# Kernel tuning notes

Measured on AMD Instinct MI355X. Metric: run time of the kernel, lower is better.

## Reference

```python
import jax, jax.numpy as jnp
import numpy as np

B, D, F, P = 65536, 256, 512, 256


def setup_inputs() -> dict:
    key = jax.random.key(0)
    k_x, k_f, k_p, k_a, k_b, k_t = jax.random.split(key, 6)
    x = jax.random.normal(k_x, (B, D), dtype=jnp.float32)
    # reset_parameters: uniform(-0.27, 1)
    features = jax.random.uniform(k_f, (F, D), dtype=jnp.float32, minval=-0.27, maxval=1.0)
    prototypes = jax.random.uniform(k_p, (P, D), dtype=jnp.float32, minval=-0.27, maxval=1.0)
    # alpha/beta/theta init to zeros in the module; use small random values so the
    # output is non-trivial for kernel correctness checking.
    alpha = jax.random.normal(k_a, (1,), dtype=jnp.float32) * 0.1
    beta = jax.random.normal(k_b, (1,), dtype=jnp.float32) * 0.1
    theta = jax.random.normal(k_t, (1,), dtype=jnp.float32) * 0.1
    return {"x": x, "features": features, "prototypes": prototypes,
            "alpha": alpha, "beta": beta, "theta": theta}


def reference(x, features, prototypes, alpha, beta, theta):
    # Shared projections
    x_features = x @ features.T                 # [B, F]
    p_features = prototypes @ features.T        # [P, F]
    x_present = jax.nn.relu(x_features)         # [B, F]
    p_present = jax.nn.relu(p_features)         # [P, F]
    x_weighted = x_features * x_present         # [B, F]
    p_weighted = p_features * p_present         # [P, F]

    # Tversky terms
    common = x_weighted @ p_weighted.T                          # [B, P]
    x_weighted_sum = jnp.sum(x_weighted, axis=1, keepdims=True)  # [B, 1]
    x_p_interaction = x_weighted @ p_present.T                  # [B, P]
    x_distinctive = x_weighted_sum - x_p_interaction            # [B, P]
    p_weighted_sum = jnp.sum(p_weighted, axis=1)[None, :]        # [1, P]
    x_p_weighted_interaction = x_present @ p_weighted.T         # [B, P]
    p_distinctive = p_weighted_sum - x_p_weighted_interaction   # [B, P]

    return theta * common - alpha * x_distinctive - beta * p_distinctive
```

## Files before the change

kernel.cpp:

```cpp
#include <hip/hip_runtime.h>
#include <cstdint>
#include <cstddef>

#define Bsz 65536
#define Dsz 256
#define Fsz 512
#define Psz 256

typedef __attribute__((ext_vector_type(8))) short short8;
typedef __attribute__((ext_vector_type(4))) short short4v;
typedef __attribute__((ext_vector_type(4))) float float4v;
typedef __attribute__((ext_vector_type(16))) float float16v;

__device__ inline short f2bf(float f) {
    unsigned u = __builtin_bit_cast(unsigned, f);
    u = (u + 0x7FFFu + ((u >> 16) & 1u)) >> 16;
    return (short)u;
}
__device__ inline float bf2f(short s) {
    unsigned u = ((unsigned)(unsigned short)s) << 16;
    return __builtin_bit_cast(float, u);
}
__device__ inline void async16(const void* g, void* l) {
    __builtin_amdgcn_global_load_lds((const __attribute__((address_space(1))) void*)g,
                                     (__attribute__((address_space(3))) void*)l, 16, 0, 0);
}

__global__ void k_prep(const float* __restrict__ features, short* __restrict__ featb,
                       float* __restrict__ pws_neg) {
    int i = blockIdx.x * 256 + threadIdx.x;
    featb[i] = f2bf(features[i]);
    if (blockIdx.x == 0) pws_neg[threadIdx.x] = 0.f;
}

#define SBPITCH 136

__global__ __launch_bounds__(256, 2) void k_pside(
    const float* __restrict__ prototypes, const short* __restrict__ featb,
    const float* __restrict__ beta_p,
    short* __restrict__ pwt, short* __restrict__ ppm1t, float* __restrict__ pws_neg)
{
    __shared__ char lds[35840];
    short* As = (short*)lds;
    short* Bs = (short*)(lds + 16384);
    short* Sb = (short*)lds;

    const int t = threadIdx.x;
    const int w = t >> 6, lane = t & 63, l15 = lane & 15, l4 = lane >> 4;
    const int rowg = blockIdx.x >> 2, nc = blockIdx.x & 3;
    const float beta = *beta_p;

    float4v acc[4][4];
    #pragma unroll
    for (int a = 0; a < 4; ++a)
        #pragma unroll
        for (int b = 0; b < 4; ++b) acc[a][b] = (float4v){0.f, 0.f, 0.f, 0.f};

    const float* pbase = prototypes + (size_t)rowg * 128 * Dsz;

    for (int kc = 0; kc < 4; ++kc) {
        __syncthreads();
        #pragma unroll
        for (int j = 0; j < 8; ++j) {
            int idx = j * 1024 + t * 4;
            int r = idx >> 6, c = idx & 63;
            float4v v = *(const float4v*)(pbase + (size_t)r * Dsz + kc * 64 + c);
            int unit = r * 8 + ((c >> 3) ^ (r & 7));
            short4v s; s.x = f2bf(v.x); s.y = f2bf(v.y); s.z = f2bf(v.z); s.w = f2bf(v.w);
            *(short4v*)((char*)As + unit * 16 + (c & 7) * 2) = s;
        }
        #pragma unroll
        for (int j = 0; j < 4; ++j) {
            int u0 = j * 256 + w * 64;
            int u = u0 + lane;
            int m = u >> 3, k8 = (u & 7) ^ (m & 7);
            async16(featb + (size_t)(nc * 128 + m) * Dsz + kc * 64 + k8 * 8, Bs + (size_t)u0 * 8);
        }
        __syncthreads();
        #pragma unroll
        for (int kk = 0; kk < 2; ++kk) {
            short8 af[4], bf[4];
            const int k8 = kk * 4 + l4;
            #pragma unroll
            for (int tm = 0; tm < 4; ++tm) {
                int m = (w & 1) * 64 + tm * 16 + l15;
                af[tm] = *(const short8*)&As[(m * 8 + (k8 ^ (m & 7))) * 8];
            }
            #pragma unroll
            for (int tn = 0; tn < 4; ++tn) {
                int n = (w >> 1) * 64 + tn * 16 + l15;
                bf[tn] = *(const short8*)&Bs[(n * 8 + (k8 ^ (n & 7))) * 8];
            }
            #pragma unroll
            for (int tm = 0; tm < 4; ++tm)
                #pragma unroll
                for (int tn = 0; tn < 4; ++tn)
                    acc[tm][tn] = __builtin_amdgcn_mfma_f32_16x16x32_bf16(af[tm], bf[tn], acc[tm][tn], 0, 0, 0);
        }
    }
    __syncthreads();
    #pragma unroll
    for (int tm = 0; tm < 4; ++tm)
        #pragma unroll
        for (int tn = 0; tn < 4; ++tn)
            #pragma unroll
            for (int r = 0; r < 4; ++r) {
                int row = (w & 1) * 64 + tm * 16 + l4 * 4 + r;
                int col = (w >> 1) * 64 + tn * 16 + l15;
                Sb[row * SBPITCH + col] = f2bf(acc[tm][tn][r]);
            }
    __syncthreads();
    #pragma unroll
    for (int rep = 0; rep < 8; ++rep) {
        int u = rep * 256 + t;
        int row = u >> 4, i = u & 15;
        short8 sv = *(const short8*)&Sb[row * SBPITCH + i * 8];
        short8 pwv, pmv;
        float sum = 0.f;
        #pragma unroll
        for (int e = 0; e < 8; ++e) {
            float pf = bf2f(sv[e]);
            float pp = fmaxf(pf, 0.f);
            float pw = pf * pp;
            pwv[e] = f2bf(pw);
            pmv[e] = f2bf(pp - 1.0f);
            sum += pw;
        }
        size_t p = (size_t)rowg * 128 + row;
        int gcol = nc * 128 + i * 8;
        *(short8*)&pwt[p * Fsz + gcol]   = pwv;
        *(short8*)&ppm1t[p * Fsz + gcol] = pmv;
        #pragma unroll
        for (int mk = 1; mk < 16; mk <<= 1) sum += __shfl_xor(sum, mk, 64);
        if ((lane & 15) == 0) atomicAdd(&pws_neg[p], -beta * sum);
    }
}

__global__ __launch_bounds__(256, 3) void k_main(
    const float* __restrict__ x, const short* __restrict__ featb,
    const short* __restrict__ pwt, const short* __restrict__ ppm1t,
    const float* __restrict__ pws_neg,
    const float* __restrict__ alpha_p, const float* __restrict__ beta_p,
    const float* __restrict__ theta_p, float* __restrict__ out)
{
    __shared__ char lds[53248];
    short* const A12 = (short*)(lds + 49152);

    const int t = threadIdx.x;
    const int w = t >> 6, lane = t & 63, l15 = lane & 15, l4 = lane >> 4;
    const int l31 = lane & 31, half = lane >> 5;
    const float alpha = *alpha_p, beta = *beta_p, theta = *theta_p;
    const size_t row0 = (size_t)blockIdx.x * 64;

    short8 xreg[8];
    {
        const float* xr = x + (row0 + 16 * w + l15) * Dsz + l4 * 8;
        #pragma unroll
        for (int kk = 0; kk < 8; ++kk) {
            float4v v0 = *(const float4v*)(xr + kk * 32);
            float4v v1 = *(const float4v*)(xr + kk * 32 + 4);
            short8 s;
            s[0] = f2bf(v0.x); s[1] = f2bf(v0.y); s[2] = f2bf(v0.z); s[3] = f2bf(v0.w);
            s[4] = f2bf(v1.x); s[5] = f2bf(v1.y); s[6] = f2bf(v1.z); s[7] = f2bf(v1.w);
            xreg[kk] = s;
        }
    }

    auto stage = [&](int kc) {
        int buf = kc & 1;
        short* FB = (short*)(lds + buf * 8192);
        short* PB = (short*)(lds + 16384 + buf * 16384);
        #pragma unroll
        for (int j = 0; j < 2; ++j) {
            int u0 = j * 256 + w * 64;
            int u = u0 + lane;
            int f = u >> 5, gg = (u & 31) ^ (f & 7);
            async16(featb + (size_t)(kc * 16 + f) * Dsz + gg * 8, FB + (size_t)u0 * 8);
        }
        #pragma unroll
        for (int j = 0; j < 4; ++j) {
            int u0 = j * 256 + w * 64;
            int u = u0 + lane;
            int p = u >> 2, sg = u & 3, g = sg ^ ((p >> 1) & 3);
            const short* src = (g < 2)
                ? pwt   + (size_t)p * Fsz + kc * 16 + g * 8
                : ppm1t + (size_t)p * Fsz + kc * 16 + (g - 2) * 8;
            async16(src, PB + (size_t)u0 * 8);
        }
    };

    float16v acc[2][2];
    #pragma unroll
    for (int a = 0; a < 2; ++a)
        #pragma unroll
        for (int b = 0; b < 2; ++b)
            #pragma unroll
            for (int e = 0; e < 16; ++e) acc[a][b][e] = 0.f;

    stage(0);

    for (int kc = 0; kc < 32; ++kc) {
        int buf = kc & 1;
        short* FBc = (short*)(lds + buf * 8192);
        short* PBc = (short*)(lds + 16384 + buf * 16384);
        __syncthreads();

        float4v s = (float4v){0.f, 0.f, 0.f, 0.f};
        #pragma unroll
        for (int kk = 0; kk < 8; ++kk) {
            int g = kk * 4 + l4;
            short8 bf = *(const short8*)&FBc[(l15 * 32 + (g ^ (l15 & 7))) * 8];
            s = __builtin_amdgcn_mfma_f32_16x16x32_bf16(xreg[kk], bf, s, 0, 0, 0);
        }
        #pragma unroll
        for (int r = 0; r < 4; ++r) {
            float sv = s[r];
            float xp = fmaxf(sv, 0.f);
            float xw = sv * xp;
            int m = 16 * w + l4 * 4 + r;
            int swz = (m >> 1) & 3;
            int u1 = m * 4 + ((l15 >> 3) ^ swz);
            int u2 = m * 4 + ((2 + (l15 >> 3)) ^ swz);
            A12[u1 * 8 + (l15 & 7)] = f2bf(theta * xw + beta * xp);
            A12[u2 * 8 + (l15 & 7)] = f2bf(alpha * xw);
        }
        __syncthreads();

        if (kc + 1 < 32) stage(kc + 1);

        short8 afr[2][2], bfr[2][2];
        #pragma unroll
        for (int mi = 0; mi < 2; ++mi)
            #pragma unroll
            for (int ks = 0; ks < 2; ++ks) {
                int m = 32 * mi + l31;
                int g = 2 * ks + half;
                afr[mi][ks] = *(const short8*)&A12[(m * 4 + (g ^ ((m >> 1) & 3))) * 8];
            }
        #pragma unroll
        for (int ni = 0; ni < 2; ++ni)
            #pragma unroll
            for (int ks = 0; ks < 2; ++ks) {
                int p = 64 * w + 32 * ni + l31;
                int g = 2 * ks + half;
                bfr[ni][ks] = *(const short8*)&PBc[(p * 4 + (g ^ ((p >> 1) & 3))) * 8];
            }
        #pragma unroll
        for (int mi = 0; mi < 2; ++mi)
            #pragma unroll
            for (int ni = 0; ni < 2; ++ni) {
                acc[mi][ni] = __builtin_amdgcn_mfma_f32_32x32x16_bf16(afr[mi][0], bfr[ni][0], acc[mi][ni], 0, 0, 0);
                acc[mi][ni] = __builtin_amdgcn_mfma_f32_32x32x16_bf16(afr[mi][1], bfr[ni][1], acc[mi][ni], 0, 0, 0);
            }
    }

    #pragma unroll
    for (int ni = 0; ni < 2; ++ni) {
        int col = 64 * w + 32 * ni + l31;
        float pn = pws_neg[col];
        #pragma unroll
        for (int mi = 0; mi < 2; ++mi)
            #pragma unroll
            for (int rg = 0; rg < 16; ++rg) {
                size_t grow = row0 + 32 * mi + (rg & 3) + 8 * (rg >> 2) + 4 * half;
                out[grow * Psz + col] = acc[mi][ni][rg] + pn;
            }
    }
}

extern "C" void kernel_launch(void* const* d_in, const int* in_sizes, int n_in,
                              void* d_out, int out_size, void* d_ws, size_t ws_size,
                              hipStream_t stream) {
    const float* x          = (const float*)d_in[0];
    const float* features   = (const float*)d_in[1];
    const float* prototypes = (const float*)d_in[2];
    const float* alpha      = (const float*)d_in[3];
    const float* beta       = (const float*)d_in[4];
    const float* theta      = (const float*)d_in[5];
    float* out = (float*)d_out;

    char* ws = (char*)d_ws;
    short* featb   = (short*)(ws);
    short* pwt     = (short*)(ws + 262144);
    short* ppm1t   = (short*)(ws + 524288);
    float* pws_neg = (float*)(ws + 786432);

    hipLaunchKernelGGL(k_prep,  dim3(512),  dim3(256), 0, stream, features, featb, pws_neg);
    hipLaunchKernelGGL(k_pside, dim3(8),    dim3(256), 0, stream, prototypes, featb, beta,
                       pwt, ppm1t, pws_neg);
    hipLaunchKernelGGL(k_main,  dim3(1024), dim3(256), 0, stream, x, featb, pwt, ppm1t,
                       pws_neg, alpha, beta, theta, out);
}
```

Baseline: 215.2 us.

## Pre-swizzle weights into MFMA fragment layout and load directly from global

The prep and prototype-side kernels now write the bf16 features and the prototype weight tables in a layout that matches the per-lane MFMA fragment order. The main kernel reads B fragments straight from global memory (L2-resident) instead of staging them through LDS with async copies. It double-buffers only the small activation tile in LDS, which lets it drop one barrier per iteration and shrink LDS use. The tradeoffs are that global-load latency is no longer hidden by an async prefetch pipeline and that every block repeatedly reads the weights from cache.

```diff
diff --git a/kernel.cpp b/kernel.cpp
--- a/kernel.cpp
+++ b/kernel.cpp
@@ -21,28 +21,32 @@
     unsigned u = ((unsigned)(unsigned short)s) << 16;
     return __builtin_bit_cast(float, u);
 }
-__device__ inline void async16(const void* g, void* l) {
-    __builtin_amdgcn_global_load_lds((const __attribute__((address_space(1))) void*)g,
-                                     (__attribute__((address_space(3))) void*)l, 16, 0, 0);
-}
-
-__global__ void k_prep(const float* __restrict__ features, short* __restrict__ featb,
+
+
+__global__ void k_prep(const float* __restrict__ features, short* __restrict__ featbB,
                        float* __restrict__ pws_neg) {
-    int i = blockIdx.x * 256 + threadIdx.x;
-    featb[i] = f2bf(features[i]);
-    if (blockIdx.x == 0) pws_neg[threadIdx.x] = 0.f;
+    int idx = blockIdx.x * 256 + threadIdx.x;
+    int f = idx >> 5, d0 = (idx & 31) * 8;
+    float4v v0 = *(const float4v*)(features + (size_t)f * Dsz + d0);
+    float4v v1 = *(const float4v*)(features + (size_t)f * Dsz + d0 + 4);
+    short8 s;
+    s[0] = f2bf(v0.x); s[1] = f2bf(v0.y); s[2] = f2bf(v0.z); s[3] = f2bf(v0.w);
+    s[4] = f2bf(v1.x); s[5] = f2bf(v1.y); s[6] = f2bf(v1.z); s[7] = f2bf(v1.w);
+    int lane = (f & 15) + 16 * ((d0 >> 3) & 3);
+    size_t o = (size_t)(f >> 4) * 4096 + (size_t)(d0 >> 5) * 512 + (size_t)lane * 8;
+    *(short8*)&featbB[o] = s;
+    if (idx < Psz) pws_neg[idx] = 0.f;
 }
 
 #define SBPITCH 136
 
 __global__ __launch_bounds__(256, 2) void k_pside(
-    const float* __restrict__ prototypes, const short* __restrict__ featb,
+    const float* __restrict__ prototypes, const short* __restrict__ featbB,
     const float* __restrict__ beta_p,
-    short* __restrict__ pwt, short* __restrict__ ppm1t, float* __restrict__ pws_neg)
+    short* __restrict__ pwB, short* __restrict__ pmB, float* __restrict__ pws_neg)
 {
     __shared__ char lds[35840];
     short* As = (short*)lds;
-    short* Bs = (short*)(lds + 16384);
     short* Sb = (short*)lds;
 
     const int t = threadIdx.x;
@@ -69,13 +73,6 @@
             short4v s; s.x = f2bf(v.x); s.y = f2bf(v.y); s.z = f2bf(v.z); s.w = f2bf(v.w);
             *(short4v*)((char*)As + unit * 16 + (c & 7) * 2) = s;
         }
-        #pragma unroll
-        for (int j = 0; j < 4; ++j) {
-            int u0 = j * 256 + w * 64;
-            int u = u0 + lane;
-            int m = u >> 3, k8 = (u & 7) ^ (m & 7);
-            async16(featb + (size_t)(nc * 128 + m) * Dsz + kc * 64 + k8 * 8, Bs + (size_t)u0 * 8);
-        }
         __syncthreads();
         #pragma unroll
         for (int kk = 0; kk < 2; ++kk) {
@@ -88,8 +85,9 @@
             }
             #pragma unroll
             for (int tn = 0; tn < 4; ++tn) {
-                int n = (w >> 1) * 64 + tn * 16 + l15;
-                bf[tn] = *(const short8*)&Bs[(n * 8 + (k8 ^ (n & 7))) * 8];
+                int fcb = nc * 8 + (w >> 1) * 4 + tn;
+                bf[tn] = *(const short8*)&featbB[(size_t)fcb * 4096 +
+                                                 (size_t)(kc * 2 + kk) * 512 + (size_t)lane * 8];
             }
             #pragma unroll
             for (int tm = 0; tm < 4; ++tm)
@@ -126,10 +124,13 @@
             pmv[e] = f2bf(pp - 1.0f);
             sum += pw;
         }
-        size_t p = (size_t)rowg * 128 + row;
+        int p = rowg * 128 + row;
         int gcol = nc * 128 + i * 8;
-        *(short8*)&pwt[p * Fsz + gcol]   = pwv;
-        *(short8*)&ppm1t[p * Fsz + gcol] = pmv;
+        size_t fo = (size_t)(gcol >> 4) * 4096 + (size_t)(p >> 6) * 1024 +
+                    (size_t)((p >> 5) & 1) * 512 +
+                    (size_t)((p & 31) + 32 * ((gcol >> 3) & 1)) * 8;
+        *(short8*)&pwB[fo] = pwv;
+        *(short8*)&pmB[fo] = pmv;
         #pragma unroll
         for (int mk = 1; mk < 16; mk <<= 1) sum += __shfl_xor(sum, mk, 64);
         if ((lane & 15) == 0) atomicAdd(&pws_neg[p], -beta * sum);
@@ -137,14 +138,13 @@
 }
 
 __global__ __launch_bounds__(256, 3) void k_main(
-    const float* __restrict__ x, const short* __restrict__ featb,
-    const short* __restrict__ pwt, const short* __restrict__ ppm1t,
+    const float* __restrict__ x, const short* __restrict__ featbB,
+    const short* __restrict__ pwB, const short* __restrict__ pmB,
     const float* __restrict__ pws_neg,
     const float* __restrict__ alpha_p, const float* __restrict__ beta_p,
     const float* __restrict__ theta_p, float* __restrict__ out)
 {
-    __shared__ char lds[53248];
-    short* const A12 = (short*)(lds + 49152);
+    __shared__ short A12[4096];
 
     const int t = threadIdx.x;
     const int w = t >> 6, lane = t & 63, l15 = lane & 15, l4 = lane >> 4;
@@ -166,29 +166,6 @@
         }
     }
 
-    auto stage = [&](int kc) {
-        int buf = kc & 1;
-        short* FB = (short*)(lds + buf * 8192);
-        short* PB = (short*)(lds + 16384 + buf * 16384);
-        #pragma unroll
-        for (int j = 0; j < 2; ++j) {
-            int u0 = j * 256 + w * 64;
-            int u = u0 + lane;
-            int f = u >> 5, gg = (u & 31) ^ (f & 7);
-            async16(featb + (size_t)(kc * 16 + f) * Dsz + gg * 8, FB + (size_t)u0 * 8);
-        }
-        #pragma unroll
-        for (int j = 0; j < 4; ++j) {
-            int u0 = j * 256 + w * 64;
-            int u = u0 + lane;
-            int p = u >> 2, sg = u & 3, g = sg ^ ((p >> 1) & 3);
-            const short* src = (g < 2)
-                ? pwt   + (size_t)p * Fsz + kc * 16 + g * 8
-                : ppm1t + (size_t)p * Fsz + kc * 16 + (g - 2) * 8;
-            async16(src, PB + (size_t)u0 * 8);
-        }
-    };
-
     float16v acc[2][2];
     #pragma unroll
     for (int a = 0; a < 2; ++a)
@@ -197,61 +174,59 @@
             #pragma unroll
             for (int e = 0; e < 16; ++e) acc[a][b][e] = 0.f;
 
-    stage(0);
-
-    for (int kc = 0; kc < 32; ++kc) {
-        int buf = kc & 1;
-        short* FBc = (short*)(lds + buf * 8192);
-        short* PBc = (short*)(lds + 16384 + buf * 16384);
-        __syncthreads();
-
-        float4v s = (float4v){0.f, 0.f, 0.f, 0.f};
-        #pragma unroll
-        for (int kk = 0; kk < 8; ++kk) {
-            int g = kk * 4 + l4;
-            short8 bf = *(const short8*)&FBc[(l15 * 32 + (g ^ (l15 & 7))) * 8];
-            s = __builtin_amdgcn_mfma_f32_16x16x32_bf16(xreg[kk], bf, s, 0, 0, 0);
-        }
+    const int mbase = 16 * w + l4 * 4;
+
+    for (int fc = 0; fc < 32; ++fc) {
+        const int buf = (fc & 1) << 11;
+
+        const short* fbase = featbB + (size_t)fc * 4096 + (size_t)lane * 8;
+        float4v s0 = (float4v){0.f, 0.f, 0.f, 0.f};
+        float4v s1 = (float4v){0.f, 0.f, 0.f, 0.f};
+        #pragma unroll
+        for (int kk = 0; kk < 8; kk += 2) {
+            short8 b0 = *(const short8*)(fbase + kk * 512);
+            short8 b1 = *(const short8*)(fbase + kk * 512 + 512);
+            s0 = __builtin_amdgcn_mfma_f32_16x16x32_bf16(xreg[kk],     b0, s0, 0, 0, 0);
+            s1 = __builtin_amdgcn_mfma_f32_16x16x32_bf16(xreg[kk + 1], b1, s1, 0, 0, 0);
+        }
+
         #pragma unroll
         for (int r = 0; r < 4; ++r) {
-            float sv = s[r];
+            float sv = s0[r] + s1[r];
             float xp = fmaxf(sv, 0.f);
             float xw = sv * xp;
-            int m = 16 * w + l4 * 4 + r;
-            int swz = (m >> 1) & 3;
+            int m = mbase + r;
+            int swz = (m >> 2) & 3;
             int u1 = m * 4 + ((l15 >> 3) ^ swz);
-            int u2 = m * 4 + ((2 + (l15 >> 3)) ^ swz);
-            A12[u1 * 8 + (l15 & 7)] = f2bf(theta * xw + beta * xp);
-            A12[u2 * 8 + (l15 & 7)] = f2bf(alpha * xw);
-        }
+            int u2 = m * 4 + ((2 | (l15 >> 3)) ^ swz);
+            A12[buf + u1 * 8 + (l15 & 7)] = f2bf(theta * xw + beta * xp);
+            A12[buf + u2 * 8 + (l15 & 7)] = f2bf(alpha * xw);
+        }
+
+        const short* pb = pwB + (size_t)fc * 4096 + (size_t)w * 1024 + (size_t)lane * 8;
+        const short* mb = pmB + (size_t)fc * 4096 + (size_t)w * 1024 + (size_t)lane * 8;
+        short8 bw0 = *(const short8*)(pb);
+        short8 bw1 = *(const short8*)(pb + 512);
+        short8 bm0 = *(const short8*)(mb);
+        short8 bm1 = *(const short8*)(mb + 512);
+
         __syncthreads();
 
-        if (kc + 1 < 32) stage(kc + 1);
-
-        short8 afr[2][2], bfr[2][2];
-        #pragma unroll
-        for (int mi = 0; mi < 2; ++mi)
-            #pragma unroll
-            for (int ks = 0; ks < 2; ++ks) {
-                int m = 32 * mi + l31;
-                int g = 2 * ks + half;
-                afr[mi][ks] = *(const short8*)&A12[(m * 4 + (g ^ ((m >> 1) & 3))) * 8];
-            }
-        #pragma unroll
-        for (int ni = 0; ni < 2; ++ni)
-            #pragma unroll
-            for (int ks = 0; ks < 2; ++ks) {
-                int p = 64 * w + 32 * ni + l31;
-                int g = 2 * ks + half;
-                bfr[ni][ks] = *(const short8*)&PBc[(p * 4 + (g ^ ((p >> 1) & 3))) * 8];
-            }
-        #pragma unroll
-        for (int mi = 0; mi < 2; ++mi)
-            #pragma unroll
-            for (int ni = 0; ni < 2; ++ni) {
-                acc[mi][ni] = __builtin_amdgcn_mfma_f32_32x32x16_bf16(afr[mi][0], bfr[ni][0], acc[mi][ni], 0, 0, 0);
-                acc[mi][ni] = __builtin_amdgcn_mfma_f32_32x32x16_bf16(afr[mi][1], bfr[ni][1], acc[mi][ni], 0, 0, 0);
-            }
+        short8 a1f[2], a2f[2];
+        #pragma unroll
+        for (int mi = 0; mi < 2; ++mi) {
+            int m = 32 * mi + l31;
+            int swz = (m >> 2) & 3;
+            a1f[mi] = *(const short8*)&A12[buf + (m * 4 + (half ^ swz)) * 8];
+            a2f[mi] = *(const short8*)&A12[buf + (m * 4 + ((2 | half) ^ swz)) * 8];
+        }
+        #pragma unroll
+        for (int mi = 0; mi < 2; ++mi) {
+            acc[mi][0] = __builtin_amdgcn_mfma_f32_32x32x16_bf16(a1f[mi], bw0, acc[mi][0], 0, 0, 0);
+            acc[mi][0] = __builtin_amdgcn_mfma_f32_32x32x16_bf16(a2f[mi], bm0, acc[mi][0], 0, 0, 0);
+            acc[mi][1] = __builtin_amdgcn_mfma_f32_32x32x16_bf16(a1f[mi], bw1, acc[mi][1], 0, 0, 0);
+            acc[mi][1] = __builtin_amdgcn_mfma_f32_32x32x16_bf16(a2f[mi], bm1, acc[mi][1], 0, 0, 0);
+        }
     }
 
     #pragma unroll
@@ -280,14 +255,14 @@
     float* out = (float*)d_out;
 
     char* ws = (char*)d_ws;
-    short* featb   = (short*)(ws);
-    short* pwt     = (short*)(ws + 262144);
-    short* ppm1t   = (short*)(ws + 524288);
+    short* featbB  = (short*)(ws);
+    short* pwB     = (short*)(ws + 262144);
+    short* pmB     = (short*)(ws + 524288);
     float* pws_neg = (float*)(ws + 786432);
 
-    hipLaunchKernelGGL(k_prep,  dim3(512),  dim3(256), 0, stream, features, featb, pws_neg);
-    hipLaunchKernelGGL(k_pside, dim3(8),    dim3(256), 0, stream, prototypes, featb, beta,
-                       pwt, ppm1t, pws_neg);
-    hipLaunchKernelGGL(k_main,  dim3(1024), dim3(256), 0, stream, x, featb, pwt, ppm1t,
+    hipLaunchKernelGGL(k_prep,  dim3(64),   dim3(256), 0, stream, features, featbB, pws_neg);
+    hipLaunchKernelGGL(k_pside, dim3(8),    dim3(256), 0, stream, prototypes, featbB, beta,
+                       pwB, pmB, pws_neg);
+    hipLaunchKernelGGL(k_main,  dim3(1024), dim3(256), 0, stream, x, featbB, pwB, pmB,
                        pws_neg, alpha, beta, theta, out);
 }
```

Result: faster. 194.8 us (-9.5%).
